# Kernel tuning notes

Hardware: AMD Instinct MI355X
Metric: run time of the kernel (lower is better)

The kernel has to match this reference:

```python
import jax, jax.numpy as jnp
import numpy as np

WS = (14, 14)
NUM_HEADS = 12
DIM = 768
HEAD_DIM = DIM // NUM_HEADS
N_TOK = WS[0] * WS[1] + 1  # 197 (cls token)
NUM_REL = (2 * WS[0] - 1) * (2 * WS[1] - 1) + 3  # 732
B = 64


def _build_rel_pos_index():
    ch, cw = np.arange(WS[0]), np.arange(WS[1])
    coords = np.stack(np.meshgrid(ch, cw, indexing='ij'))  # [2,h,w]
    cf = coords.reshape(2, -1)  # [2, h*w]
    rel = cf[:, :, None] - cf[:, None, :]  # [2, hw, hw]
    rel = rel.transpose(1, 2, 0).astype(np.int64)
    rel[:, :, 0] += WS[0] - 1
    rel[:, :, 1] += WS[1] - 1
    rel[:, :, 0] *= 2 * WS[1] - 1
    idx = np.zeros((N_TOK, N_TOK), dtype=np.int64)
    idx[1:, 1:] = rel.sum(-1)
    idx[0, 0:] = NUM_REL - 3
    idx[0:, 0] = NUM_REL - 2
    idx[0, 0] = NUM_REL - 1
    return idx.astype(np.int32)


def setup_inputs() -> dict:
    key = jax.random.key(0)
    ks = jax.random.split(key, 7)
    s = 0.02
    return {
        'x': jax.random.normal(ks[0], (B, N_TOK, DIM), jnp.float32),
        'qkv_w': jax.random.normal(ks[1], (3 * DIM, DIM), jnp.float32) * s,
        'q_bias': jax.random.normal(ks[2], (DIM,), jnp.float32) * s,
        'v_bias': jax.random.normal(ks[3], (DIM,), jnp.float32) * s,
        'rpb_table': jax.random.normal(ks[4], (NUM_REL, NUM_HEADS), jnp.float32) * s,
        'proj_w': jax.random.normal(ks[5], (DIM, DIM), jnp.float32) * s,
        'proj_b': jax.random.normal(ks[6], (DIM,), jnp.float32) * s,
        'rel_pos_index': jnp.asarray(_build_rel_pos_index()),
    }


def reference(x, qkv_w, q_bias, v_bias, rpb_table, proj_w, proj_b, rel_pos_index):
    Bb, N, C = x.shape
    scale = HEAD_DIM ** -0.5
    # qkv bias: [q_bias, zeros(k), v_bias]
    qkv_bias = jnp.concatenate([q_bias, jnp.zeros_like(v_bias), v_bias])
    qkv = x @ qkv_w.T + qkv_bias  # [B,N,3C]
    qkv = qkv.reshape(Bb, N, 3, NUM_HEADS, HEAD_DIM).transpose(2, 0, 3, 1, 4)
    q, k, v = qkv[0], qkv[1], qkv[2]  # [B,H,N,hd]
    attn = jnp.einsum('bhnd,bhmd->bhnm', q * scale, k)
    # gather relative position bias: [N,N,H] -> [1,H,N,N]
    rpb = rpb_table[rel_pos_index]  # [N,N,H]
    attn = attn + rpb.transpose(2, 0, 1)[None]
    attn = jax.nn.softmax(attn, axis=-1)
    out = jnp.einsum('bhnm,bhmd->bhnd', attn, v)
    out = out.transpose(0, 2, 1, 3).reshape(Bb, N, NUM_HEADS * HEAD_DIM)
    return out @ proj_w.T + proj_b
```

## Files before the change

### kernel.cpp

```cpp
#include <hip/hip_runtime.h>
#include <hip/hip_bf16.h>
#include <cstdint>
#include <cstddef>

typedef __bf16 bf16x8 __attribute__((ext_vector_type(8)));
typedef float f32x4 __attribute__((ext_vector_type(4)));

#define DI __device__ __forceinline__
#define AS1 __attribute__((address_space(1)))
#define AS3 __attribute__((address_space(3)))

DI unsigned short f2bf(float x) {
    union { float f; unsigned int u; } v; v.f = x;
    unsigned int u = v.u;
    u += 0x7FFFu + ((u >> 16) & 1u);
    return (unsigned short)(u >> 16);
}

#define BATCH 64
#define NH 12
#define NTOK 197
#define NTOK_P 208
#define HD 64
#define DIM 768
#define MROWS 12608
#define MPAD 224
#define PLDS2 236
#define CPAD 132
#define QSCALE 0.18033688f
#define LOG2E 1.4426950408889634f

DI int xcd_swz(int orig, int nwg) {
    int q = nwg >> 3, r = nwg & 7;
    int x = orig & 7, l = orig >> 3;
    return (x < r ? x * (q + 1) : r * (q + 1) + (x - r) * q) + l;
}

DI int swz(int row, int col_elem) {
    return (row * 64 + col_elem) ^ ((row & 7) << 3);
}


__global__ void cvt3_bf16_kernel(const float* __restrict__ a, unsigned short* __restrict__ oa, int na4,
                                 const float* __restrict__ b, unsigned short* __restrict__ ob, int nb4,
                                 const float* __restrict__ c, unsigned short* __restrict__ oc, int nc4) {
    int i = blockIdx.x * blockDim.x + threadIdx.x;
    const float* src; unsigned short* dst; int k;
    if (i < na4) { src = a; dst = oa; k = i; }
    else if (i < na4 + nb4) { src = b; dst = ob; k = i - na4; }
    else if (i < na4 + nb4 + nc4) { src = c; dst = oc; k = i - na4 - nb4; }
    else return;
    float4 f = ((const float4*)src)[k];
    ushort4 o;
    o.x = f2bf(f.x); o.y = f2bf(f.y); o.z = f2bf(f.z); o.w = f2bf(f.w);
    ((ushort4*)dst)[k] = o;
}

__global__ void build_rpb2_kernel(const float* __restrict__ table, const int* __restrict__ idx,
                                  float* __restrict__ out) {
    int i = blockIdx.x * blockDim.x + threadIdx.x;
    if (i >= NH * 7 * 13 * 512) return;
    int j = i & 3;
    int g = (i >> 2) & 1;
    int lane = (i >> 3) & 63;
    int rest = i >> 9;
    int t = rest % 13;
    int qt = (rest / 13) % 7;
    int h = rest / 91;
    int row = qt * 32 + g * 16 + ((lane >> 4) << 2) + j;
    int col = t * 16 + (lane & 15);
    float v = 0.f;
    if (row < NTOK && col < NTOK) v = table[idx[row * NTOK + col] * NH + h] * LOG2E;
    out[i] = v;
}

__global__ void zero_vt_pad_kernel(unsigned short* __restrict__ vt) {
    const int npad = MPAD - NTOK;
    int i = blockIdx.x * blockDim.x + threadIdx.x;
    if (i >= BATCH * NH * HD * npad) return;
    int c = NTOK + (i % npad);
    int row = i / npad;
    vt[(size_t)row * MPAD + c] = 0;
}


template<int EPI>
__launch_bounds__(256)
__global__ void gemm_bt_kernel(const unsigned short* __restrict__ A,
                               const unsigned short* __restrict__ W,
                               const float* __restrict__ bias0,
                               const float* __restrict__ bias1,
                               void* __restrict__ out0,
                               unsigned short* __restrict__ out1,
                               unsigned short* __restrict__ out2,
                               int M, int ntiles)
{
    __shared__ __align__(16) unsigned short smem[32768];
    const int K = DIM;
    const int NT = K / 64;
    int wgid = xcd_swz(blockIdx.x, gridDim.x);
    int mt = wgid / ntiles, nt = wgid % ntiles;
    int m0 = mt * 128, n0 = nt * 128;
    int tid = threadIdx.x;
    int lane = tid & 63, w = tid >> 6;
    int wr = (w >> 1) * 64, wc = (w & 1) * 64;

    const int st_row = lane >> 3;
    const int st_col = ((lane & 7) ^ (lane >> 3)) << 3;

    f32x4 acc[4][4] = {};

    auto stage = [&](int buf, int ks) {
        unsigned short* as = smem + buf * 8192;
        unsigned short* bs = smem + 16384 + buf * 8192;
#pragma unroll
        for (int i = 0; i < 4; i++) {
            int s = w * 4 + i;
            int arow = m0 + s * 8 + st_row; if (arow >= M) arow = M - 1;
            __builtin_amdgcn_global_load_lds(
                (const AS1 void*)(A + (size_t)arow * K + ks + st_col),
                (AS3 void*)(as + s * 512), 16, 0, 0);
        }
#pragma unroll
        for (int i = 0; i < 4; i++) {
            int s = w * 4 + i;
            __builtin_amdgcn_global_load_lds(
                (const AS1 void*)(W + (size_t)(n0 + s * 8 + st_row) * K + ks + st_col),
                (AS3 void*)(bs + s * 512), 16, 0, 0);
        }
    };

    stage(0, 0);
    __syncthreads();
    int cur = 0;
    for (int t = 0; t < NT; ++t) {
        if (t + 1 < NT) stage(cur ^ 1, (t + 1) * 64);
        const unsigned short* as = smem + cur * 8192;
        const unsigned short* bs = smem + 16384 + cur * 8192;
#pragma unroll
        for (int kc = 0; kc < 2; kc++) {
            bf16x8 af[4], bfr[4];
#pragma unroll
            for (int x = 0; x < 4; x++)
                af[x] = *(const bf16x8*)&as[swz(wr + x * 16 + (lane & 15), kc * 32 + (lane >> 4) * 8)];
#pragma unroll
            for (int y = 0; y < 4; y++)
                bfr[y] = *(const bf16x8*)&bs[swz(wc + y * 16 + (lane & 15), kc * 32 + (lane >> 4) * 8)];
#pragma unroll
            for (int x = 0; x < 4; x++)
#pragma unroll
                for (int y = 0; y < 4; y++)
                    acc[x][y] = __builtin_amdgcn_mfma_f32_16x16x32_bf16(af[x], bfr[y], acc[x][y], 0, 0, 0);
        }
        __syncthreads();
        cur ^= 1;
    }

    if constexpr (EPI == 1) {
#pragma unroll
        for (int x = 0; x < 4; x++)
#pragma unroll
            for (int y = 0; y < 4; y++)
#pragma unroll
                for (int j = 0; j < 4; j++) {
                    int m = m0 + wr + x * 16 + (lane >> 4) * 4 + j;
                    int n = n0 + wc + y * 16 + (lane & 15);
                    if (m < M)
                        ((float*)out0)[(size_t)m * DIM + n] = acc[x][y][j] + bias0[n];
                }
    } else {
        int which = n0 / DIM;
        int hn0 = n0 - which * DIM;
        unsigned short* lc = smem;

#pragma unroll
        for (int x = 0; x < 4; x++)
#pragma unroll
            for (int y = 0; y < 4; y++)
#pragma unroll
                for (int j = 0; j < 4; j++) {
                    int ml = wr + x * 16 + (lane >> 4) * 4 + j;
                    int nl = wc + y * 16 + (lane & 15);
                    float val = acc[x][y][j];
                    if (which == 0) val = (val + bias0[hn0 + nl]) * QSCALE;
                    else if (which == 2) val = val + bias1[hn0 + nl];
                    lc[ml * CPAD + nl] = f2bf(val);
                }
        __syncthreads();

        if (which != 2) {
            unsigned short* outq = (which == 0) ? (unsigned short*)out0 : out1;
            int c4 = (lane & 31) * 4;
            int h = (hn0 >> 6) + (c4 >> 6), d = c4 & 63;
            for (int it = 0; it < 16; ++it) {
                int r = it * 8 + w * 2 + (lane >> 5);
                int m = m0 + r;
                if (m >= M) continue;
                int b = m / NTOK, t = m - b * NTOK;
                ushort4 q4 = *(const ushort4*)&lc[r * CPAD + c4];
                *(ushort4*)&outq[(((size_t)b * NH + h) * NTOK_P + t) * HD + d] = q4;
            }
        } else {
            int mh = w >> 1, hs = w & 1;
            int h = (hn0 >> 6) + hs;
            int ml = mh * 64 + lane;
            int m = m0 + ml;
            if (m < M) {
                int b = m / NTOK, t = m - b * NTOK;
                unsigned short* vbase = out2 + (((size_t)b * NH + h) * HD) * MPAD + t;
#pragma unroll 8
                for (int d = 0; d < 64; ++d)
                    vbase[(size_t)d * MPAD] = lc[ml * CPAD + hs * 64 + d];
            }
        }
    }
}


__launch_bounds__(64)
__global__ void attn_kernel(const unsigned short* __restrict__ qbuf,
                            const unsigned short* __restrict__ kbuf,
                            const unsigned short* __restrict__ vt,
                            const float* __restrict__ rpb2,
                            unsigned short* __restrict__ ao)
{
    __shared__ __align__(16) unsigned short p_lds[32][PLDS2];
    int bid = xcd_swz(blockIdx.x, gridDim.x);
    int qt = bid % 7, bh = bid / 7;
    int b = bh / NH, h = bh - b * NH;
    int lane = threadIdx.x;
    int r0 = qt * 32;
    int col_l = lane & 15, hi = lane >> 4;

    {
        int rr = lane >> 1, cc = NTOK_P + (lane & 1) * 8;
        ushort4 z = {0, 0, 0, 0};
        *(ushort4*)&p_lds[rr][cc] = z;
        *(ushort4*)&p_lds[rr][cc + 4] = z;
    }

    const size_t kqbase = (size_t)bh * NTOK_P * HD;
    int qr0 = r0 + col_l;      if (qr0 > NTOK_P - 1) qr0 = NTOK_P - 1;
    int qr1 = r0 + 16 + col_l; if (qr1 > NTOK_P - 1) qr1 = NTOK_P - 1;
    bf16x8 qf0a = *(const bf16x8*)&qbuf[kqbase + (size_t)qr0 * HD + hi * 8];
    bf16x8 qf0b = *(const bf16x8*)&qbuf[kqbase + (size_t)qr0 * HD + 32 + hi * 8];
    bf16x8 qf1a = *(const bf16x8*)&qbuf[kqbase + (size_t)qr1 * HD + hi * 8];
    bf16x8 qf1b = *(const bf16x8*)&qbuf[kqbase + (size_t)qr1 * HD + 32 + hi * 8];

    const float* rpbase = rpb2 + ((size_t)(h * 7 + qt) * 13) * 512 + lane * 8;

    float lrow[2][4] = {};
#pragma unroll
    for (int t = 0; t < 13; t++) {
        int krow = t * 16 + col_l;
        bf16x8 kf0 = *(const bf16x8*)&kbuf[kqbase + (size_t)krow * HD + hi * 8];
        bf16x8 kf1 = *(const bf16x8*)&kbuf[kqbase + (size_t)krow * HD + 32 + hi * 8];
        f32x4 z = {0.f, 0.f, 0.f, 0.f};
        f32x4 sA = __builtin_amdgcn_mfma_f32_16x16x32_bf16(qf0a, kf0, z, 0, 0, 0);
        sA = __builtin_amdgcn_mfma_f32_16x16x32_bf16(qf0b, kf1, sA, 0, 0, 0);
        f32x4 sB = __builtin_amdgcn_mfma_f32_16x16x32_bf16(qf1a, kf0, z, 0, 0, 0);
        sB = __builtin_amdgcn_mfma_f32_16x16x32_bf16(qf1b, kf1, sB, 0, 0, 0);
        float4 ra = *(const float4*)&rpbase[(size_t)t * 512];
        float4 rb = *(const float4*)&rpbase[(size_t)t * 512 + 4];
        float raj[4] = {ra.x, ra.y, ra.z, ra.w};
        float rbj[4] = {rb.x, rb.y, rb.z, rb.w};
        bool masked = (t * 16 + col_l >= NTOK);
#pragma unroll
        for (int j = 0; j < 4; j++) {
            float vA = sA[j] + raj[j];
            float vB = sB[j] + rbj[j];
            if (masked) { vA = -1e30f; vB = -1e30f; }
            float pA = exp2f(vA);
            float pB = exp2f(vB);
            lrow[0][j] += pA;
            lrow[1][j] += pB;
            p_lds[hi * 4 + j][t * 16 + col_l] = f2bf(pA);
            p_lds[16 + hi * 4 + j][t * 16 + col_l] = f2bf(pB);
        }
    }
    float inv[2][4];
#pragma unroll
    for (int g = 0; g < 2; g++)
#pragma unroll
        for (int j = 0; j < 4; j++) {
            float lv = lrow[g][j];
            lv += __shfl_xor(lv, 1);
            lv += __shfl_xor(lv, 2);
            lv += __shfl_xor(lv, 4);
            lv += __shfl_xor(lv, 8);
            inv[g][j] = __builtin_amdgcn_rcpf(lv);
        }

    f32x4 o[2][4] = {};
    const size_t vbase = (size_t)bh * HD * MPAD;
    __builtin_amdgcn_s_setprio(1);
#pragma unroll
    for (int c = 0; c < 7; c++) {
        bf16x8 pf0 = *(const bf16x8*)&p_lds[col_l][c * 32 + hi * 8];
        bf16x8 pf1 = *(const bf16x8*)&p_lds[16 + col_l][c * 32 + hi * 8];
#pragma unroll
        for (int n = 0; n < 4; n++) {
            bf16x8 vf = *(const bf16x8*)&vt[vbase + (size_t)(n * 16 + col_l) * MPAD + c * 32 + hi * 8];
            o[0][n] = __builtin_amdgcn_mfma_f32_16x16x32_bf16(pf0, vf, o[0][n], 0, 0, 0);
            o[1][n] = __builtin_amdgcn_mfma_f32_16x16x32_bf16(pf1, vf, o[1][n], 0, 0, 0);
        }
    }
    __builtin_amdgcn_s_setprio(0);

#pragma unroll
    for (int g = 0; g < 2; g++)
#pragma unroll
        for (int n = 0; n < 4; n++)
#pragma unroll
            for (int j = 0; j < 4; j++) {
                int tok = r0 + g * 16 + hi * 4 + j;
                if (tok < NTOK) {
                    float val = o[g][n][j] * inv[g][j];
                    ao[((size_t)b * NTOK + tok) * DIM + h * HD + n * 16 + col_l] = f2bf(val);
                }
            }
}


extern "C" void kernel_launch(void* const* d_in, const int* in_sizes, int n_in,
                              void* d_out, int out_size, void* d_ws, size_t ws_size,
                              hipStream_t stream)
{
    const float* x      = (const float*)d_in[0];
    const float* qkv_w  = (const float*)d_in[1];
    const float* q_bias = (const float*)d_in[2];
    const float* v_bias = (const float*)d_in[3];
    const float* rpb_t  = (const float*)d_in[4];
    const float* proj_w = (const float*)d_in[5];
    const float* proj_b = (const float*)d_in[6];
    const int*   relidx = (const int*)d_in[7];
    float* out = (float*)d_out;

    char* ws = (char*)d_ws;
    const size_t SZ_XBF  = (size_t)MROWS * DIM * 2;
    const size_t SZ_QKVW = (size_t)3 * DIM * DIM * 2;
    const size_t SZ_PRJW = (size_t)DIM * DIM * 2;
    const size_t SZ_QK   = (size_t)BATCH * NH * NTOK_P * HD * 2;
    const size_t SZ_VT   = (size_t)BATCH * NH * HD * MPAD * 2;

    unsigned short* x_bf = (unsigned short*)ws;
    unsigned short* ao   = x_bf;
    size_t off = SZ_XBF;
    unsigned short* qkvw_bf  = (unsigned short*)(ws + off); off += SZ_QKVW;
    unsigned short* projw_bf = (unsigned short*)(ws + off); off += SZ_PRJW;
    unsigned short* qbuf     = (unsigned short*)(ws + off); off += SZ_QK;
    unsigned short* kbuf     = (unsigned short*)(ws + off); off += SZ_QK;
    unsigned short* vtbuf    = (unsigned short*)(ws + off); off += SZ_VT;
    float* rpbf              = (float*)(ws + off);

    const int NA4 = MROWS * DIM / 4, NB4 = 3 * DIM * DIM / 4, NC4 = DIM * DIM / 4;
    cvt3_bf16_kernel<<<(NA4 + NB4 + NC4 + 255) / 256, 256, 0, stream>>>(
        x, x_bf, NA4, qkv_w, qkvw_bf, NB4, proj_w, projw_bf, NC4);
    build_rpb2_kernel<<<(NH * 7 * 13 * 512 + 255) / 256, 256, 0, stream>>>(rpb_t, relidx, rpbf);
    zero_vt_pad_kernel<<<(BATCH * NH * HD * (MPAD - NTOK) + 255) / 256, 256, 0, stream>>>(vtbuf);

    gemm_bt_kernel<0><<<99 * 18, 256, 0, stream>>>(x_bf, qkvw_bf, q_bias, v_bias,
                                                   (void*)qbuf, kbuf, vtbuf, MROWS, 18);
    attn_kernel<<<BATCH * NH * 7, 64, 0, stream>>>(qbuf, kbuf, vtbuf, rpbf, ao);
    gemm_bt_kernel<1><<<99 * 6, 256, 0, stream>>>(ao, projw_bf, proj_b, nullptr,
                                                  (void*)out, nullptr, nullptr, MROWS, 6);
    (void)in_sizes; (void)n_in; (void)out_size; (void)ws_size;
}
```

Before: 185.3 us.

## Switch GEMMs to 256x256 tiles with 512 threads and explicit double-buffered waits

Both GEMMs now use 256x256 output tiles computed by 8 waves with K-step 32, a new LDS swizzle, and a two-stage prefetch synchronised by explicit vmcnt waits and barriers. MFMA issue is bracketed by s_setprio. The QKV epilogue writes the tile out in four 64-row quarters through LDS to fit shared memory. The larger tile raises data reuse per load, but it cuts the grid to 450 and 150 workgroups, which risks poor CU occupancy on the output projection (150 blocks on a 256-CU part).

```diff
diff --git a/kernel.cpp b/kernel.cpp
--- a/kernel.cpp
+++ b/kernel.cpp
@@ -26,7 +26,7 @@
 #define MROWS 12608
 #define MPAD 224
 #define PLDS2 236
-#define CPAD 132
+#define CP2 268
 #define QSCALE 0.18033688f
 #define LOG2E 1.4426950408889634f
 
@@ -36,8 +36,8 @@
     return (x < r ? x * (q + 1) : r * (q + 1) + (x - r) * q) + l;
 }
 
-DI int swz(int row, int col_elem) {
-    return (row * 64 + col_elem) ^ ((row & 7) << 3);
+DI int pk32(int r, int k) {
+    return r * 32 + ((((k >> 3) ^ ((r >> 2) & 3)) << 3) | (k & 7));
 }
 
 
@@ -85,8 +85,8 @@
 
 
 template<int EPI>
-__launch_bounds__(256)
-__global__ void gemm_bt_kernel(const unsigned short* __restrict__ A,
+__launch_bounds__(512)
+__global__ void gemm256_kernel(const unsigned short* __restrict__ A,
                                const unsigned short* __restrict__ W,
                                const float* __restrict__ bias0,
                                const float* __restrict__ bias1,
@@ -97,120 +97,137 @@
 {
     __shared__ __align__(16) unsigned short smem[32768];
     const int K = DIM;
-    const int NT = K / 64;
+    const int NT = 24;
     int wgid = xcd_swz(blockIdx.x, gridDim.x);
     int mt = wgid / ntiles, nt = wgid % ntiles;
-    int m0 = mt * 128, n0 = nt * 128;
-    int tid = threadIdx.x;
-    int lane = tid & 63, w = tid >> 6;
-    int wr = (w >> 1) * 64, wc = (w & 1) * 64;
-
-    const int st_row = lane >> 3;
-    const int st_col = ((lane & 7) ^ (lane >> 3)) << 3;
-
-    f32x4 acc[4][4] = {};
+    int m0 = mt * 256, n0 = nt * 256;
+    int tid = threadIdx.x, lane = tid & 63, w = tid >> 6;
+    int wm = w >> 2, wn = w & 3;
+    int r15 = lane & 15, hi = lane >> 4, hi8 = hi * 8;
+
+    f32x4 acc[8][4] = {};
+
+    const int st_row = tid >> 2;
+    const int st_kk  = (((tid & 3) ^ ((tid >> 4) & 3)) << 3);
 
     auto stage = [&](int buf, int ks) {
         unsigned short* as = smem + buf * 8192;
         unsigned short* bs = smem + 16384 + buf * 8192;
 #pragma unroll
-        for (int i = 0; i < 4; i++) {
-            int s = w * 4 + i;
-            int arow = m0 + s * 8 + st_row; if (arow >= M) arow = M - 1;
+        for (int i = 0; i < 2; ++i) {
+            int arow = m0 + i * 128 + st_row; if (arow >= M) arow = M - 1;
             __builtin_amdgcn_global_load_lds(
-                (const AS1 void*)(A + (size_t)arow * K + ks + st_col),
-                (AS3 void*)(as + s * 512), 16, 0, 0);
-        }
-#pragma unroll
-        for (int i = 0; i < 4; i++) {
-            int s = w * 4 + i;
+                (const AS1 void*)(A + (size_t)arow * K + ks + st_kk),
+                (AS3 void*)(as + i * 4096 + w * 512), 16, 0, 0);
             __builtin_amdgcn_global_load_lds(
-                (const AS1 void*)(W + (size_t)(n0 + s * 8 + st_row) * K + ks + st_col),
-                (AS3 void*)(bs + s * 512), 16, 0, 0);
+                (const AS1 void*)(W + (size_t)(n0 + i * 128 + st_row) * K + ks + st_kk),
+                (AS3 void*)(bs + i * 4096 + w * 512), 16, 0, 0);
         }
     };
 
     stage(0, 0);
-    __syncthreads();
-    int cur = 0;
+    stage(1, 32);
+    asm volatile("s_waitcnt vmcnt(4)" ::: "memory");
+    __builtin_amdgcn_sched_barrier(0);
+    __builtin_amdgcn_s_barrier();
+
     for (int t = 0; t < NT; ++t) {
-        if (t + 1 < NT) stage(cur ^ 1, (t + 1) * 64);
-        const unsigned short* as = smem + cur * 8192;
-        const unsigned short* bs = smem + 16384 + cur * 8192;
-#pragma unroll
-        for (int kc = 0; kc < 2; kc++) {
-            bf16x8 af[4], bfr[4];
-#pragma unroll
-            for (int x = 0; x < 4; x++)
-                af[x] = *(const bf16x8*)&as[swz(wr + x * 16 + (lane & 15), kc * 32 + (lane >> 4) * 8)];
-#pragma unroll
-            for (int y = 0; y < 4; y++)
-                bfr[y] = *(const bf16x8*)&bs[swz(wc + y * 16 + (lane & 15), kc * 32 + (lane >> 4) * 8)];
-#pragma unroll
-            for (int x = 0; x < 4; x++)
-#pragma unroll
-                for (int y = 0; y < 4; y++)
-                    acc[x][y] = __builtin_amdgcn_mfma_f32_16x16x32_bf16(af[x], bfr[y], acc[x][y], 0, 0, 0);
-        }
-        __syncthreads();
-        cur ^= 1;
+        const unsigned short* as = smem + (t & 1) * 8192;
+        const unsigned short* bs = smem + 16384 + (t & 1) * 8192;
+        bf16x8 af[8], bfr[4];
+#pragma unroll
+        for (int m = 0; m < 8; m++)
+            af[m] = *(const bf16x8*)&as[pk32(wm * 128 + m * 16 + r15, hi8)];
+#pragma unroll
+        for (int n = 0; n < 4; n++)
+            bfr[n] = *(const bf16x8*)&bs[pk32(wn * 64 + n * 16 + r15, hi8)];
+        __builtin_amdgcn_s_setprio(1);
+#pragma unroll
+        for (int m = 0; m < 8; m++)
+#pragma unroll
+            for (int n = 0; n < 4; n++)
+                acc[m][n] = __builtin_amdgcn_mfma_f32_16x16x32_bf16(af[m], bfr[n], acc[m][n], 0, 0, 0);
+        __builtin_amdgcn_s_setprio(0);
+        asm volatile("s_waitcnt lgkmcnt(0)" ::: "memory");
+        __builtin_amdgcn_sched_barrier(0);
+        __builtin_amdgcn_s_barrier();
+        if (t + 2 < NT) {
+            stage(t & 1, (t + 2) * 32);
+            asm volatile("s_waitcnt vmcnt(4)" ::: "memory");
+        } else {
+            asm volatile("s_waitcnt vmcnt(0)" ::: "memory");
+        }
+        __builtin_amdgcn_sched_barrier(0);
+        __builtin_amdgcn_s_barrier();
     }
 
     if constexpr (EPI == 1) {
 #pragma unroll
-        for (int x = 0; x < 4; x++)
-#pragma unroll
-            for (int y = 0; y < 4; y++)
+        for (int m = 0; m < 8; m++)
+#pragma unroll
+            for (int n = 0; n < 4; n++)
 #pragma unroll
                 for (int j = 0; j < 4; j++) {
-                    int m = m0 + wr + x * 16 + (lane >> 4) * 4 + j;
-                    int n = n0 + wc + y * 16 + (lane & 15);
-                    if (m < M)
-                        ((float*)out0)[(size_t)m * DIM + n] = acc[x][y][j] + bias0[n];
+                    int row = m0 + wm * 128 + m * 16 + hi * 4 + j;
+                    int col = n0 + wn * 64 + n * 16 + r15;
+                    if (row < M)
+                        ((float*)out0)[(size_t)row * DIM + col] = acc[m][n][j] + bias0[col];
                 }
     } else {
-        int which = n0 / DIM;
-        int hn0 = n0 - which * DIM;
+        int which = nt / 3, part = nt % 3, hb = part * 4;
         unsigned short* lc = smem;
 
 #pragma unroll
-        for (int x = 0; x < 4; x++)
-#pragma unroll
-            for (int y = 0; y < 4; y++)
-#pragma unroll
-                for (int j = 0; j < 4; j++) {
-                    int ml = wr + x * 16 + (lane >> 4) * 4 + j;
-                    int nl = wc + y * 16 + (lane & 15);
-                    float val = acc[x][y][j];
-                    if (which == 0) val = (val + bias0[hn0 + nl]) * QSCALE;
-                    else if (which == 2) val = val + bias1[hn0 + nl];
-                    lc[ml * CPAD + nl] = f2bf(val);
-                }
-        __syncthreads();
-
-        if (which != 2) {
-            unsigned short* outq = (which == 0) ? (unsigned short*)out0 : out1;
-            int c4 = (lane & 31) * 4;
-            int h = (hn0 >> 6) + (c4 >> 6), d = c4 & 63;
-            for (int it = 0; it < 16; ++it) {
-                int r = it * 8 + w * 2 + (lane >> 5);
-                int m = m0 + r;
-                if (m >= M) continue;
-                int b = m / NTOK, t = m - b * NTOK;
-                ushort4 q4 = *(const ushort4*)&lc[r * CPAD + c4];
-                *(ushort4*)&outq[(((size_t)b * NH + h) * NTOK_P + t) * HD + d] = q4;
+        for (int qd = 0; qd < 4; ++qd) {
+            __syncthreads();
+            if (wm == (qd >> 1)) {
+#pragma unroll
+                for (int mm = 0; mm < 4; mm++) {
+                    int m = (qd & 1) * 4 + mm;
+#pragma unroll
+                    for (int n = 0; n < 4; n++)
+#pragma unroll
+                        for (int j = 0; j < 4; j++) {
+                            int lrow = mm * 16 + hi * 4 + j;
+                            int col = wn * 64 + n * 16 + r15;
+                            float val = acc[m][n][j];
+                            int gcol = part * 256 + col;
+                            if (which == 0) val = (val + bias0[gcol]) * QSCALE;
+                            else if (which == 2) val = val + bias1[gcol];
+                            lc[lrow * CP2 + col] = f2bf(val);
+                        }
+                }
             }
-        } else {
-            int mh = w >> 1, hs = w & 1;
-            int h = (hn0 >> 6) + hs;
-            int ml = mh * 64 + lane;
-            int m = m0 + ml;
-            if (m < M) {
-                int b = m / NTOK, t = m - b * NTOK;
-                unsigned short* vbase = out2 + (((size_t)b * NH + h) * HD) * MPAD + t;
-#pragma unroll 8
-                for (int d = 0; d < 64; ++d)
-                    vbase[(size_t)d * MPAD] = lc[ml * CPAD + hs * 64 + d];
+            __syncthreads();
+
+            if (which != 2) {
+                unsigned short* dst = (which == 0) ? (unsigned short*)out0 : out1;
+#pragma unroll
+                for (int it = 0; it < 8; ++it) {
+                    int flat = it * 32 + w * 4 + hi;
+                    int hh = flat >> 6, r = flat & 63;
+                    int m = m0 + qd * 64 + r;
+                    if (m < M) {
+                        int b = m / NTOK, tk = m - b * NTOK;
+                        ushort4 u = *(const ushort4*)&lc[r * CP2 + hh * 64 + r15 * 4];
+                        *(ushort4*)&dst[(((size_t)b * NH + hb + hh) * NTOK_P + tk) * HD + r15 * 4] = u;
+                    }
+                }
+            } else {
+                int m = m0 + qd * 64 + lane;
+                if (m < M) {
+                    int b = m / NTOK, tk = m - b * NTOK;
+                    size_t obase = ((size_t)b * NH + hb) * HD * MPAD + tk;
+#pragma unroll
+                    for (int dd = 0; dd < 16; ++dd) {
+                        int col = w * 32 + dd * 2;
+                        int hh = col >> 6, d = col & 63;
+                        unsigned int u = *(const unsigned int*)&lc[lane * CP2 + col];
+                        unsigned short* vb = out2 + obase + ((size_t)hh * HD + d) * MPAD;
+                        vb[0] = (unsigned short)(u & 0xffffu);
+                        vb[MPAD] = (unsigned short)(u >> 16);
+                    }
+                }
             }
         }
     }
@@ -359,10 +376,10 @@
     build_rpb2_kernel<<<(NH * 7 * 13 * 512 + 255) / 256, 256, 0, stream>>>(rpb_t, relidx, rpbf);
     zero_vt_pad_kernel<<<(BATCH * NH * HD * (MPAD - NTOK) + 255) / 256, 256, 0, stream>>>(vtbuf);
 
-    gemm_bt_kernel<0><<<99 * 18, 256, 0, stream>>>(x_bf, qkvw_bf, q_bias, v_bias,
-                                                   (void*)qbuf, kbuf, vtbuf, MROWS, 18);
+    gemm256_kernel<0><<<50 * 9, 512, 0, stream>>>(x_bf, qkvw_bf, q_bias, v_bias,
+                                                  (void*)qbuf, kbuf, vtbuf, MROWS, 9);
     attn_kernel<<<BATCH * NH * 7, 64, 0, stream>>>(qbuf, kbuf, vtbuf, rpbf, ao);
-    gemm_bt_kernel<1><<<99 * 6, 256, 0, stream>>>(ao, projw_bf, proj_b, nullptr,
-                                                  (void*)out, nullptr, nullptr, MROWS, 6);
+    gemm256_kernel<1><<<50 * 3, 512, 0, stream>>>(ao, projw_bf, proj_b, nullptr,
+                                                  (void*)out, nullptr, nullptr, MROWS, 3);
     (void)in_sizes; (void)n_in; (void)out_size; (void)ws_size;
 }
```

Result: slower. 211.7 us, median of 2 (+14.2%).
